# Optimization experiments

Measured on AMD Instinct MI355X. Metric: run time of the kernel, lower is better.

The kernel has to match this reference:

```python
import jax, jax.numpy as jnp
import numpy as np
from jax import lax

ITER, L, D, H = 8, 4096, 512, 256


def setup_inputs() -> dict:
    key = jax.random.key(0)
    ks = jax.random.split(key, 12)
    sD = 1.0 / np.sqrt(D)
    sH = 1.0 / np.sqrt(H)
    return {
        "embeddings_seq": jax.random.normal(ks[0], (ITER, L, D), jnp.float32),
        "ROIs": jax.random.uniform(ks[1], (1, L, 3), jnp.float32),
        "Wx": jax.random.normal(ks[2], (L, D), jnp.float32) * sD,
        "bx": jax.random.normal(ks[3], (L,), jnp.float32) * 0.01,
        "Wy": jax.random.normal(ks[4], (L, D), jnp.float32) * sD,
        "by": jax.random.normal(ks[5], (L,), jnp.float32) * 0.01,
        "Wz": jax.random.normal(ks[6], (L, D), jnp.float32) * sD,
        "bz": jax.random.normal(ks[7], (L,), jnp.float32) * 0.01,
        "Ws": jax.random.normal(ks[8], (D, H), jnp.float32) * sD,
        "bs": jax.random.normal(ks[9], (H,), jnp.float32) * 0.01,
        "Wh": jax.random.normal(ks[10], (L, H), jnp.float32) * sH,
        "bh": jax.random.normal(ks[11], (L,), jnp.float32) * 0.01,
    }


def reference(embeddings_seq, ROIs, Wx, bx, Wy, by, Wz, bz, Ws, bs, Wh, bh):
    # size_tensor = [1/767, 1/767, 1/575]
    size = jnp.array([1.0 / 767, 1.0 / 767, 1.0 / 575], dtype=embeddings_seq.dtype)

    def dec(h):  # grouped Conv1d(k=D, groups=L) == per-landmark dot product; h: [L, D]
        x = jnp.sum(Wx * h, axis=-1) + bx
        y = jnp.sum(Wy * h, axis=-1) + by
        z = jnp.sum(Wz * h, axis=-1) + bz
        return jnp.stack([x, y, z], axis=-1)  # [L, 3]

    def gate_head(h):  # Linear+Tanh shared, then per-landmark grouped conv; h: [L, D]
        s = jnp.tanh(h @ Ws + bs)          # [L, H]
        return jnp.sum(Wh * s, axis=-1) + bh  # [L]

    emb0 = embeddings_seq[0]                  # [L, D]
    rois0 = ROIs[0]                           # [L, 3]
    predict0 = dec(emb0) * size + rois0       # [L, 3]

    def step(carry, emb):
        h, c, pred = carry
        rois = pred                           # previous prediction becomes new ROIs
        gf = gate_head(h)                     # [L]
        ga = gate_head(emb)                   # [L]
        g = jax.nn.softmax(jnp.stack([gf, ga], axis=-1), axis=-1)  # [L, 2]
        g0, g1 = g[:, 0:1], g[:, 1:2]
        h = h * g0 + emb * g1
        c = c * g0 + rois * g1
        pred = dec(h) * size + lax.stop_gradient(c)
        return (h, c, pred), pred

    init = (emb0, rois0, predict0)
    _, preds = lax.scan(step, init, embeddings_seq[1:])  # [ITER-1, L, 3]
    return jnp.concatenate([predict0[None], preds], axis=0)  # [ITER, L, 3]
```

## Files before the change

### kernel.cpp

```cpp
#include <hip/hip_runtime.h>
#include <stdint.h>

#define L_DIM 4096
#define D_DIM 512
#define H_DIM 256
#define T_DIM 8

typedef short bf16x8 __attribute__((ext_vector_type(8)));
typedef float f32x4 __attribute__((ext_vector_type(4)));

__device__ __forceinline__ unsigned short f2bf(float f) {
    union { float f; unsigned int u; } c; c.f = f;
    unsigned int u = c.u;
    unsigned int r = (u + 0x7fffu + ((u >> 16) & 1u)) >> 16;
    return (unsigned short)r;
}

__device__ __forceinline__ float bits2f(unsigned int u) {
    union { unsigned int u; float f; } c; c.u = u; return c.f;
}

__device__ __forceinline__ float4 unpack_bf4(uint2 q) {
    float4 r;
    r.x = bits2f(q.x << 16);
    r.y = bits2f(q.x & 0xffff0000u);
    r.z = bits2f(q.y << 16);
    r.w = bits2f(q.y & 0xffff0000u);
    return r;
}

__device__ __forceinline__ float wave_sum(float x) {
    #pragma unroll
    for (int off = 32; off > 0; off >>= 1) x += __shfl_xor(x, off, 64);
    return x;
}

__device__ __forceinline__ float dot4(float4 a, float4 b) {
    return a.x * b.x + a.y * b.y + a.z * b.z + a.w * b.w;
}

__device__ __forceinline__ float fast_tanh(float x) {
    float e = __expf(2.0f * x);
    return 1.0f - 2.0f / (e + 1.0f);
}

__device__ __forceinline__ float4 tanh4b(float4 a, float4 b) {
    float4 r;
    r.x = fast_tanh(a.x + b.x); r.y = fast_tanh(a.y + b.y);
    r.z = fast_tanh(a.z + b.z); r.w = fast_tanh(a.w + b.w);
    return r;
}

__global__ void k_transpose_ws(const float* __restrict__ Ws,
                               unsigned short* __restrict__ WsT) {
    int idx = blockIdx.x * 256 + threadIdx.x;
    int j = idx >> 9;
    int k = idx & 511;
    WsT[idx] = f2bf(Ws[k * H_DIM + j]);
}

__global__ __launch_bounds__(512, 4) void k_fused(
    const float* __restrict__ emb, const float* __restrict__ rois,
    const float* __restrict__ Wx, const float* __restrict__ bx,
    const float* __restrict__ Wy, const float* __restrict__ by,
    const float* __restrict__ Wz, const float* __restrict__ bz,
    const float* __restrict__ bs, const float* __restrict__ Wh,
    const float* __restrict__ bh, const unsigned short* __restrict__ WsT,
    float* __restrict__ out) {
    __shared__ __align__(16) char smem[81920];

    const int tid  = threadIdx.x;
    const int lane = tid & 63;
    const int wid  = tid >> 6;
    const int wm   = wid >> 2;
    const int wn   = wid & 3;
    const int lbase = blockIdx.x * 8;

    const int arow = tid >> 4, aq = tid & 15;
    const int t0 = arow >> 3, li0 = arow & 7;
    const float* ag0 = emb + ((long)t0 * L_DIM + lbase + li0) * D_DIM + aq * 4;
    const float* ag1 = ag0 + (long)4 * L_DIM * D_DIM;
    const int adst0 = arow * 128 + ((aq * 8) ^ ((arow & 7) << 4));
    const int adst1 = (arow + 32) * 128 + ((aq * 8) ^ (((arow + 32) & 7) << 4));
    const int bj = tid >> 3, bko = tid & 7;
    const unsigned short* bg = WsT + (long)bj * D_DIM + bko * 8;
    const int bdst[4] = {
        bj * 128 + ((bko * 16) ^ ((bj & 7) << 4)),
        (bj + 64) * 128 + ((bko * 16) ^ (((bj + 64) & 7) << 4)),
        (bj + 128) * 128 + ((bko * 16) ^ (((bj + 128) & 7) << 4)),
        (bj + 192) * 128 + ((bko * 16) ^ (((bj + 192) & 7) << 4))};

    f32x4 acc[2][4];
    #pragma unroll
    for (int mi = 0; mi < 2; mi++)
        #pragma unroll
        for (int ni = 0; ni < 4; ni++) acc[mi][ni] = (f32x4){0.f, 0.f, 0.f, 0.f};

    {
        float4 a0 = *(const float4*)(ag0);
        float4 a1 = *(const float4*)(ag1);
        char* As = smem;
        char* Bs = smem + 8192;
        uint2 p0, p1;
        p0.x = (unsigned)f2bf(a0.x) | ((unsigned)f2bf(a0.y) << 16);
        p0.y = (unsigned)f2bf(a0.z) | ((unsigned)f2bf(a0.w) << 16);
        p1.x = (unsigned)f2bf(a1.x) | ((unsigned)f2bf(a1.y) << 16);
        p1.y = (unsigned)f2bf(a1.z) | ((unsigned)f2bf(a1.w) << 16);
        *(uint2*)(As + adst0) = p0;
        *(uint2*)(As + adst1) = p1;
        #pragma unroll
        for (int p = 0; p < 4; p++)
            *(uint4*)(Bs + bdst[p]) = *(const uint4*)(bg + (long)p * 64 * D_DIM);
    }
    __syncthreads();

    #pragma unroll
    for (int kt = 0; kt < 8; ++kt) {
        char* As = smem + (kt & 1) * 40960;
        char* Bs = As + 8192;
        char* Asn = smem + ((kt + 1) & 1) * 40960;
        char* Bsn = Asn + 8192;

        float4 a0, a1;
        uint4 b0, b1, b2, b3;
        if (kt < 7) {
            const float* ap0 = ag0 + (kt + 1) * 64;
            const float* ap1 = ag1 + (kt + 1) * 64;
            a0 = *(const float4*)(ap0);
            a1 = *(const float4*)(ap1);
            const unsigned short* bp = bg + (kt + 1) * 64;
            b0 = *(const uint4*)(bp);
            b1 = *(const uint4*)(bp + (long)64 * D_DIM);
            b2 = *(const uint4*)(bp + (long)128 * D_DIM);
            b3 = *(const uint4*)(bp + (long)192 * D_DIM);
        }

        #pragma unroll
        for (int ks = 0; ks < 2; ++ks) {
            bf16x8 a[2], b[4];
            #pragma unroll
            for (int mi = 0; mi < 2; mi++) {
                int row = wm * 32 + mi * 16 + (lane & 15);
                a[mi] = *(const bf16x8*)(As + row * 128 +
                          (((ks * 64) + (lane >> 4) * 16) ^ ((row & 7) << 4)));
            }
            #pragma unroll
            for (int ni = 0; ni < 4; ni++) {
                int j = wn * 64 + ni * 16 + (lane & 15);
                b[ni] = *(const bf16x8*)(Bs + j * 128 +
                          (((ks * 64) + (lane >> 4) * 16) ^ ((j & 7) << 4)));
            }
            #pragma unroll
            for (int mi = 0; mi < 2; mi++)
                #pragma unroll
                for (int ni = 0; ni < 4; ni++)
                    acc[mi][ni] = __builtin_amdgcn_mfma_f32_16x16x32_bf16(
                        a[mi], b[ni], acc[mi][ni], 0, 0, 0);
        }

        if (kt < 7) {
            uint2 p0, p1;
            p0.x = (unsigned)f2bf(a0.x) | ((unsigned)f2bf(a0.y) << 16);
            p0.y = (unsigned)f2bf(a0.z) | ((unsigned)f2bf(a0.w) << 16);
            p1.x = (unsigned)f2bf(a1.x) | ((unsigned)f2bf(a1.y) << 16);
            p1.y = (unsigned)f2bf(a1.z) | ((unsigned)f2bf(a1.w) << 16);
            *(uint2*)(Asn + adst0) = p0;
            *(uint2*)(Asn + adst1) = p1;
            *(uint4*)(Bsn + bdst[0]) = b0;
            *(uint4*)(Bsn + bdst[1]) = b1;
            *(uint4*)(Bsn + bdst[2]) = b2;
            *(uint4*)(Bsn + bdst[3]) = b3;
        }
        __syncthreads();
    }

    unsigned short* v_lds = (unsigned short*)smem;
    #pragma unroll
    for (int mi = 0; mi < 2; mi++)
        #pragma unroll
        for (int ni = 0; ni < 4; ni++)
            #pragma unroll
            for (int r = 0; r < 4; r++) {
                int row = wm * 32 + mi * 16 + (lane >> 4) * 4 + r;
                int col = wn * 64 + ni * 16 + (lane & 15);
                v_lds[row * H_DIM + col] = f2bf(acc[mi][ni][r]);
            }
    __syncthreads();

    const int l = lbase + wid;
    const int j4 = lane * 4;
    const int d8 = lane * 8;

    float4 Wh4 = *(const float4*)(Wh + (long)l * H_DIM + j4);
    float4 bs4 = *(const float4*)(bs + j4);
    float4 wx0 = *(const float4*)(Wx + (long)l * D_DIM + d8);
    float4 wx1 = *(const float4*)(Wx + (long)l * D_DIM + d8 + 4);
    float4 wy0 = *(const float4*)(Wy + (long)l * D_DIM + d8);
    float4 wy1 = *(const float4*)(Wy + (long)l * D_DIM + d8 + 4);
    float4 wz0 = *(const float4*)(Wz + (long)l * D_DIM + d8);
    float4 wz1 = *(const float4*)(Wz + (long)l * D_DIM + d8 + 4);
    float bxl = bx[l], byl = by[l], bzl = bz[l], bhl = bh[l];
    const float sx = 1.f / 767.f, sy = 1.f / 767.f, sz = 1.f / 575.f;

    uint2 vvp[T_DIM];
    #pragma unroll
    for (int t = 0; t < T_DIM; ++t)
        vvp[t] = *(const uint2*)(v_lds + (t * 8 + wid) * H_DIM + j4);

    float px[T_DIM], py[T_DIM], pz[T_DIM], ga[T_DIM];
    #pragma unroll
    for (int t = 0; t < T_DIM; ++t) {
        const float* eb = emb + ((long)t * L_DIM + l) * D_DIM + d8;
        float4 f0 = *(const float4*)(eb);
        float4 f1 = *(const float4*)(eb + 4);
        px[t] = dot4(wx0, f0) + dot4(wx1, f1);
        py[t] = dot4(wy0, f0) + dot4(wy1, f1);
        pz[t] = dot4(wz0, f0) + dot4(wz1, f1);
        float4 sa = tanh4b(unpack_bf4(vvp[t]), bs4);
        ga[t] = dot4(Wh4, sa);
    }
    #pragma unroll
    for (int t = 0; t < T_DIM; ++t) {
        px[t] = wave_sum(px[t]);
        py[t] = wave_sum(py[t]);
        pz[t] = wave_sum(pz[t]);
        ga[t] = wave_sum(ga[t]) + bhl;
    }

    float4 u4 = unpack_bf4(vvp[0]);
    float cx = rois[l * 3 + 0], cy = rois[l * 3 + 1], cz = rois[l * 3 + 2];
    float dx = px[0], dy = py[0], dz = pz[0];
    float prx = (dx + bxl) * sx + cx;
    float pry = (dy + byl) * sy + cy;
    float prz = (dz + bzl) * sz + cz;
    if (lane == 0) {
        out[l * 3 + 0] = prx; out[l * 3 + 1] = pry; out[l * 3 + 2] = prz;
    }

    #pragma unroll
    for (int t = 1; t < T_DIM; ++t) {
        float4 sf = tanh4b(u4, bs4);
        float gf = wave_sum(dot4(Wh4, sf)) + bhl;

        float g0 = 1.0f / (1.0f + __expf(ga[t] - gf));
        float g1 = 1.0f - g0;

        float4 v4 = unpack_bf4(vvp[t]);
        u4.x = g0 * u4.x + g1 * v4.x; u4.y = g0 * u4.y + g1 * v4.y;
        u4.z = g0 * u4.z + g1 * v4.z; u4.w = g0 * u4.w + g1 * v4.w;

        cx = cx * g0 + prx * g1; cy = cy * g0 + pry * g1; cz = cz * g0 + prz * g1;
        dx = g0 * dx + g1 * px[t]; dy = g0 * dy + g1 * py[t]; dz = g0 * dz + g1 * pz[t];

        prx = (dx + bxl) * sx + cx;
        pry = (dy + byl) * sy + cy;
        prz = (dz + bzl) * sz + cz;
        if (lane == 0) {
            float* o = out + (long)t * (L_DIM * 3) + l * 3;
            o[0] = prx; o[1] = pry; o[2] = prz;
        }
    }
}

extern "C" void kernel_launch(void* const* d_in, const int* in_sizes, int n_in,
                              void* d_out, int out_size, void* d_ws, size_t ws_size,
                              hipStream_t stream) {
    const float* emb  = (const float*)d_in[0];
    const float* rois = (const float*)d_in[1];
    const float* Wx   = (const float*)d_in[2];
    const float* bx   = (const float*)d_in[3];
    const float* Wy   = (const float*)d_in[4];
    const float* by   = (const float*)d_in[5];
    const float* Wz   = (const float*)d_in[6];
    const float* bz   = (const float*)d_in[7];
    const float* Ws   = (const float*)d_in[8];
    const float* bs   = (const float*)d_in[9];
    const float* Wh   = (const float*)d_in[10];
    const float* bh   = (const float*)d_in[11];
    float* out = (float*)d_out;

    unsigned short* WsT = (unsigned short*)d_ws;

    hipLaunchKernelGGL(k_transpose_ws, dim3(512), dim3(256), 0, stream, Ws, WsT);
    hipLaunchKernelGGL(k_fused, dim3(512), dim3(512), 0, stream,
                       emb, rois, Wx, bx, Wy, by, Wz, bz, bs, Wh, bh, WsT, out);
}
```

Baseline: 153.8 us.

## Stage full bf16 embedding tile in LDS and reuse it for decoder dot products

The kernel now loads each block's whole 64x512 embedding tile into LDS as bf16 up front, instead of streaming it per k-step alongside the Ws tile. The epilogue reads these bf16 values from LDS rather than re-reading fp32 embeddings from global memory. This removes the second global pass over the embeddings. In exchange, LDS grows to 128KB, which allows fewer resident blocks per CU. The A-operand load is no longer overlapped with compute, and the decoder and gating math now use bf16-rounded embeddings, which lowers precision.

```diff
diff --git a/kernel.cpp b/kernel.cpp
--- a/kernel.cpp
+++ b/kernel.cpp
@@ -14,6 +14,10 @@
     unsigned int u = c.u;
     unsigned int r = (u + 0x7fffu + ((u >> 16) & 1u)) >> 16;
     return (unsigned short)r;
+}
+
+__device__ __forceinline__ unsigned int pack2(float a, float b) {
+    return (unsigned)f2bf(a) | ((unsigned)f2bf(b) << 16);
 }
 
 __device__ __forceinline__ float bits2f(unsigned int u) {
@@ -59,7 +63,7 @@
     WsT[idx] = f2bf(Ws[k * H_DIM + j]);
 }
 
-__global__ __launch_bounds__(512, 4) void k_fused(
+__global__ __launch_bounds__(512, 2) void k_fused(
     const float* __restrict__ emb, const float* __restrict__ rois,
     const float* __restrict__ Wx, const float* __restrict__ bx,
     const float* __restrict__ Wy, const float* __restrict__ by,
@@ -67,7 +71,7 @@
     const float* __restrict__ bs, const float* __restrict__ Wh,
     const float* __restrict__ bh, const unsigned short* __restrict__ WsT,
     float* __restrict__ out) {
-    __shared__ __align__(16) char smem[81920];
+    __shared__ __align__(16) char smem[131072];
 
     const int tid  = threadIdx.x;
     const int lane = tid & 63;
@@ -76,12 +80,6 @@
     const int wn   = wid & 3;
     const int lbase = blockIdx.x * 8;
 
-    const int arow = tid >> 4, aq = tid & 15;
-    const int t0 = arow >> 3, li0 = arow & 7;
-    const float* ag0 = emb + ((long)t0 * L_DIM + lbase + li0) * D_DIM + aq * 4;
-    const float* ag1 = ag0 + (long)4 * L_DIM * D_DIM;
-    const int adst0 = arow * 128 + ((aq * 8) ^ ((arow & 7) << 4));
-    const int adst1 = (arow + 32) * 128 + ((aq * 8) ^ (((arow + 32) & 7) << 4));
     const int bj = tid >> 3, bko = tid & 7;
     const unsigned short* bg = WsT + (long)bj * D_DIM + bko * 8;
     const int bdst[4] = {
@@ -90,44 +88,46 @@
         (bj + 128) * 128 + ((bko * 16) ^ (((bj + 128) & 7) << 4)),
         (bj + 192) * 128 + ((bko * 16) ^ (((bj + 192) & 7) << 4))};
 
+    {
+        const int row = tid >> 3;
+        const int oct = tid & 7;
+        const int t0 = row >> 3, li0 = row & 7;
+        const float* asrc = emb + ((long)t0 * L_DIM + lbase + li0) * D_DIM + oct * 64;
+        float4 ebuf[16];
+        #pragma unroll
+        for (int q = 0; q < 16; ++q) ebuf[q] = *(const float4*)(asrc + q * 4);
+
+        char* Bs0 = smem + 65536;
+        #pragma unroll
+        for (int p = 0; p < 4; p++)
+            *(uint4*)(Bs0 + bdst[p]) = *(const uint4*)(bg + (long)p * 64 * D_DIM);
+
+        const int row7 = (row & 7) << 4;
+        #pragma unroll
+        for (int c = 0; c < 8; ++c) {
+            uint4 w;
+            w.x = pack2(ebuf[2 * c].x, ebuf[2 * c].y);
+            w.y = pack2(ebuf[2 * c].z, ebuf[2 * c].w);
+            w.z = pack2(ebuf[2 * c + 1].x, ebuf[2 * c + 1].y);
+            w.w = pack2(ebuf[2 * c + 1].z, ebuf[2 * c + 1].w);
+            *(uint4*)(smem + row * 1024 + ((((oct * 8 + c) * 16)) ^ row7)) = w;
+        }
+    }
+    __syncthreads();
+
     f32x4 acc[2][4];
     #pragma unroll
     for (int mi = 0; mi < 2; mi++)
         #pragma unroll
         for (int ni = 0; ni < 4; ni++) acc[mi][ni] = (f32x4){0.f, 0.f, 0.f, 0.f};
 
-    {
-        float4 a0 = *(const float4*)(ag0);
-        float4 a1 = *(const float4*)(ag1);
-        char* As = smem;
-        char* Bs = smem + 8192;
-        uint2 p0, p1;
-        p0.x = (unsigned)f2bf(a0.x) | ((unsigned)f2bf(a0.y) << 16);
-        p0.y = (unsigned)f2bf(a0.z) | ((unsigned)f2bf(a0.w) << 16);
-        p1.x = (unsigned)f2bf(a1.x) | ((unsigned)f2bf(a1.y) << 16);
-        p1.y = (unsigned)f2bf(a1.z) | ((unsigned)f2bf(a1.w) << 16);
-        *(uint2*)(As + adst0) = p0;
-        *(uint2*)(As + adst1) = p1;
-        #pragma unroll
-        for (int p = 0; p < 4; p++)
-            *(uint4*)(Bs + bdst[p]) = *(const uint4*)(bg + (long)p * 64 * D_DIM);
-    }
-    __syncthreads();
-
     #pragma unroll
     for (int kt = 0; kt < 8; ++kt) {
-        char* As = smem + (kt & 1) * 40960;
-        char* Bs = As + 8192;
-        char* Asn = smem + ((kt + 1) & 1) * 40960;
-        char* Bsn = Asn + 8192;
-
-        float4 a0, a1;
+        char* Bs  = smem + 65536 + (kt & 1) * 32768;
+        char* Bsn = smem + 65536 + ((kt + 1) & 1) * 32768;
+
         uint4 b0, b1, b2, b3;
         if (kt < 7) {
-            const float* ap0 = ag0 + (kt + 1) * 64;
-            const float* ap1 = ag1 + (kt + 1) * 64;
-            a0 = *(const float4*)(ap0);
-            a1 = *(const float4*)(ap1);
             const unsigned short* bp = bg + (kt + 1) * 64;
             b0 = *(const uint4*)(bp);
             b1 = *(const uint4*)(bp + (long)64 * D_DIM);
@@ -141,8 +141,9 @@
             #pragma unroll
             for (int mi = 0; mi < 2; mi++) {
                 int row = wm * 32 + mi * 16 + (lane & 15);
-                a[mi] = *(const bf16x8*)(As + row * 128 +
-                          (((ks * 64) + (lane >> 4) * 16) ^ ((row & 7) << 4)));
+                int chunk = kt * 8 + ks * 4 + (lane >> 4);
+                a[mi] = *(const bf16x8*)(smem + row * 1024 +
+                          ((chunk * 16) ^ ((row & 7) << 4)));
             }
             #pragma unroll
             for (int ni = 0; ni < 4; ni++) {
@@ -159,13 +160,6 @@
         }
 
         if (kt < 7) {
-            uint2 p0, p1;
-            p0.x = (unsigned)f2bf(a0.x) | ((unsigned)f2bf(a0.y) << 16);
-            p0.y = (unsigned)f2bf(a0.z) | ((unsigned)f2bf(a0.w) << 16);
-            p1.x = (unsigned)f2bf(a1.x) | ((unsigned)f2bf(a1.y) << 16);
-            p1.y = (unsigned)f2bf(a1.z) | ((unsigned)f2bf(a1.w) << 16);
-            *(uint2*)(Asn + adst0) = p0;
-            *(uint2*)(Asn + adst1) = p1;
             *(uint4*)(Bsn + bdst[0]) = b0;
             *(uint4*)(Bsn + bdst[1]) = b1;
             *(uint4*)(Bsn + bdst[2]) = b2;
@@ -174,7 +168,7 @@
         __syncthreads();
     }
 
-    unsigned short* v_lds = (unsigned short*)smem;
+    unsigned short* v_lds = (unsigned short*)(smem + 65536);
     #pragma unroll
     for (int mi = 0; mi < 2; mi++)
         #pragma unroll
@@ -189,10 +183,10 @@
 
     const int l = lbase + wid;
     const int j4 = lane * 4;
-    const int d8 = lane * 8;
 
     float4 Wh4 = *(const float4*)(Wh + (long)l * H_DIM + j4);
     float4 bs4 = *(const float4*)(bs + j4);
+    const int d8 = lane * 8;
     float4 wx0 = *(const float4*)(Wx + (long)l * D_DIM + d8);
     float4 wx1 = *(const float4*)(Wx + (long)l * D_DIM + d8 + 4);
     float4 wy0 = *(const float4*)(Wy + (long)l * D_DIM + d8);
@@ -210,9 +204,11 @@
     float px[T_DIM], py[T_DIM], pz[T_DIM], ga[T_DIM];
     #pragma unroll
     for (int t = 0; t < T_DIM; ++t) {
-        const float* eb = emb + ((long)t * L_DIM + l) * D_DIM + d8;
-        float4 f0 = *(const float4*)(eb);
-        float4 f1 = *(const float4*)(eb + 4);
+        int r = t * 8 + wid;
+        uint4 ev = *(const uint4*)(smem + r * 1024 +
+                     ((lane * 16) ^ ((r & 7) << 4)));
+        float4 f0 = unpack_bf4(make_uint2(ev.x, ev.y));
+        float4 f1 = unpack_bf4(make_uint2(ev.z, ev.w));
         px[t] = dot4(wx0, f0) + dot4(wx1, f1);
         py[t] = dot4(wy0, f0) + dot4(wy1, f1);
         pz[t] = dot4(wz0, f0) + dot4(wz1, f1);
```

Measured after the change: 160.2 us. 4.1% more time.

## Fuse xyz decoder dot products into GEMM A-tile load and single-buffer Ws

Applied to the files above, without the earlier changes.

Computes the Wx/Wy/Wz per-landmark dot products from the fp32 embedding values already loaded for the GEMM A tile, so the second full read of the embeddings in the epilogue is removed. Partial sums are reduced over 16-lane groups and passed through LDS. The Ws B tile becomes single-buffered with an extra barrier per k-step, which cuts LDS use from 80KB to 48KB so more blocks can be resident per CU. The cost is two barriers per iteration, extra global loads of Wx/Wy/Wz inside the main loop, and a changed fp32 summation order for the decoder outputs.

```diff
diff --git a/kernel.cpp b/kernel.cpp
--- a/kernel.cpp
+++ b/kernel.cpp
@@ -14,6 +14,10 @@
     unsigned int u = c.u;
     unsigned int r = (u + 0x7fffu + ((u >> 16) & 1u)) >> 16;
     return (unsigned short)r;
+}
+
+__device__ __forceinline__ unsigned int pack2(float a, float b) {
+    return (unsigned)f2bf(a) | ((unsigned)f2bf(b) << 16);
 }
 
 __device__ __forceinline__ float bits2f(unsigned int u) {
@@ -32,6 +36,12 @@
 __device__ __forceinline__ float wave_sum(float x) {
     #pragma unroll
     for (int off = 32; off > 0; off >>= 1) x += __shfl_xor(x, off, 64);
+    return x;
+}
+
+__device__ __forceinline__ float group16_sum(float x) {
+    #pragma unroll
+    for (int off = 8; off > 0; off >>= 1) x += __shfl_xor(x, off, 64);
     return x;
 }
 
@@ -67,7 +77,8 @@
     const float* __restrict__ bs, const float* __restrict__ Wh,
     const float* __restrict__ bh, const unsigned short* __restrict__ WsT,
     float* __restrict__ out) {
-    __shared__ __align__(16) char smem[81920];
+    __shared__ __align__(16) char smem[49152];
+    char* Bs = smem + 16384;
 
     const int tid  = threadIdx.x;
     const int lane = tid & 63;
@@ -82,6 +93,10 @@
     const float* ag1 = ag0 + (long)4 * L_DIM * D_DIM;
     const int adst0 = arow * 128 + ((aq * 8) ^ ((arow & 7) << 4));
     const int adst1 = (arow + 32) * 128 + ((aq * 8) ^ (((arow + 32) & 7) << 4));
+    const float* wxg = Wx + (long)(lbase + li0) * D_DIM + aq * 4;
+    const float* wyg = Wy + (long)(lbase + li0) * D_DIM + aq * 4;
+    const float* wzg = Wz + (long)(lbase + li0) * D_DIM + aq * 4;
+
     const int bj = tid >> 3, bko = tid & 7;
     const unsigned short* bg = WsT + (long)bj * D_DIM + bko * 8;
     const int bdst[4] = {
@@ -90,6 +105,9 @@
         (bj + 128) * 128 + ((bko * 16) ^ (((bj + 128) & 7) << 4)),
         (bj + 192) * 128 + ((bko * 16) ^ (((bj + 192) & 7) << 4))};
 
+    float pxa0 = 0.f, pya0 = 0.f, pza0 = 0.f;
+    float pxa1 = 0.f, pya1 = 0.f, pza1 = 0.f;
+
     f32x4 acc[2][4];
     #pragma unroll
     for (int mi = 0; mi < 2; mi++)
@@ -99,40 +117,41 @@
     {
         float4 a0 = *(const float4*)(ag0);
         float4 a1 = *(const float4*)(ag1);
-        char* As = smem;
-        char* Bs = smem + 8192;
-        uint2 p0, p1;
-        p0.x = (unsigned)f2bf(a0.x) | ((unsigned)f2bf(a0.y) << 16);
-        p0.y = (unsigned)f2bf(a0.z) | ((unsigned)f2bf(a0.w) << 16);
-        p1.x = (unsigned)f2bf(a1.x) | ((unsigned)f2bf(a1.y) << 16);
-        p1.y = (unsigned)f2bf(a1.z) | ((unsigned)f2bf(a1.w) << 16);
-        *(uint2*)(As + adst0) = p0;
-        *(uint2*)(As + adst1) = p1;
+        float4 wx = *(const float4*)(wxg);
+        float4 wy = *(const float4*)(wyg);
+        float4 wz = *(const float4*)(wzg);
         #pragma unroll
         for (int p = 0; p < 4; p++)
             *(uint4*)(Bs + bdst[p]) = *(const uint4*)(bg + (long)p * 64 * D_DIM);
+        pxa0 += dot4(wx, a0); pya0 += dot4(wy, a0); pza0 += dot4(wz, a0);
+        pxa1 += dot4(wx, a1); pya1 += dot4(wy, a1); pza1 += dot4(wz, a1);
+        uint2 p0, p1;
+        p0.x = pack2(a0.x, a0.y); p0.y = pack2(a0.z, a0.w);
+        p1.x = pack2(a1.x, a1.y); p1.y = pack2(a1.z, a1.w);
+        *(uint2*)(smem + adst0) = p0;
+        *(uint2*)(smem + adst1) = p1;
     }
     __syncthreads();
 
     #pragma unroll
     for (int kt = 0; kt < 8; ++kt) {
-        char* As = smem + (kt & 1) * 40960;
-        char* Bs = As + 8192;
-        char* Asn = smem + ((kt + 1) & 1) * 40960;
-        char* Bsn = Asn + 8192;
-
-        float4 a0, a1;
+        char* As  = smem + (kt & 1) * 8192;
+        char* Asn = smem + ((kt + 1) & 1) * 8192;
+
+        float4 a0, a1, wx, wy, wz;
         uint4 b0, b1, b2, b3;
         if (kt < 7) {
-            const float* ap0 = ag0 + (kt + 1) * 64;
-            const float* ap1 = ag1 + (kt + 1) * 64;
-            a0 = *(const float4*)(ap0);
-            a1 = *(const float4*)(ap1);
-            const unsigned short* bp = bg + (kt + 1) * 64;
+            const int o = (kt + 1) * 64;
+            a0 = *(const float4*)(ag0 + o);
+            a1 = *(const float4*)(ag1 + o);
+            const unsigned short* bp = bg + o;
             b0 = *(const uint4*)(bp);
             b1 = *(const uint4*)(bp + (long)64 * D_DIM);
             b2 = *(const uint4*)(bp + (long)128 * D_DIM);
             b3 = *(const uint4*)(bp + (long)192 * D_DIM);
+            wx = *(const float4*)(wxg + o);
+            wy = *(const float4*)(wyg + o);
+            wz = *(const float4*)(wzg + o);
         }
 
         #pragma unroll
@@ -159,22 +178,26 @@
         }
 
         if (kt < 7) {
+            pxa0 += dot4(wx, a0); pya0 += dot4(wy, a0); pza0 += dot4(wz, a0);
+            pxa1 += dot4(wx, a1); pya1 += dot4(wy, a1); pza1 += dot4(wz, a1);
             uint2 p0, p1;
-            p0.x = (unsigned)f2bf(a0.x) | ((unsigned)f2bf(a0.y) << 16);
-            p0.y = (unsigned)f2bf(a0.z) | ((unsigned)f2bf(a0.w) << 16);
-            p1.x = (unsigned)f2bf(a1.x) | ((unsigned)f2bf(a1.y) << 16);
-            p1.y = (unsigned)f2bf(a1.z) | ((unsigned)f2bf(a1.w) << 16);
+            p0.x = pack2(a0.x, a0.y); p0.y = pack2(a0.z, a0.w);
+            p1.x = pack2(a1.x, a1.y); p1.y = pack2(a1.z, a1.w);
             *(uint2*)(Asn + adst0) = p0;
             *(uint2*)(Asn + adst1) = p1;
-            *(uint4*)(Bsn + bdst[0]) = b0;
-            *(uint4*)(Bsn + bdst[1]) = b1;
-            *(uint4*)(Bsn + bdst[2]) = b2;
-            *(uint4*)(Bsn + bdst[3]) = b3;
         }
         __syncthreads();
-    }
-
-    unsigned short* v_lds = (unsigned short*)smem;
+        if (kt < 7) {
+            *(uint4*)(Bs + bdst[0]) = b0;
+            *(uint4*)(Bs + bdst[1]) = b1;
+            *(uint4*)(Bs + bdst[2]) = b2;
+            *(uint4*)(Bs + bdst[3]) = b3;
+        }
+        __syncthreads();
+    }
+
+    unsigned short* v_lds = (unsigned short*)(smem + 16384);
+    float* p_lds = (float*)smem;
     #pragma unroll
     for (int mi = 0; mi < 2; mi++)
         #pragma unroll
@@ -185,47 +208,40 @@
                 int col = wn * 64 + ni * 16 + (lane & 15);
                 v_lds[row * H_DIM + col] = f2bf(acc[mi][ni][r]);
             }
+    pxa0 = group16_sum(pxa0); pya0 = group16_sum(pya0); pza0 = group16_sum(pza0);
+    pxa1 = group16_sum(pxa1); pya1 = group16_sum(pya1); pza1 = group16_sum(pza1);
+    if ((lane & 15) == 0) {
+        p_lds[arow * 4 + 0] = pxa0;
+        p_lds[arow * 4 + 1] = pya0;
+        p_lds[arow * 4 + 2] = pza0;
+        p_lds[(arow + 32) * 4 + 0] = pxa1;
+        p_lds[(arow + 32) * 4 + 1] = pya1;
+        p_lds[(arow + 32) * 4 + 2] = pza1;
+    }
     __syncthreads();
 
     const int l = lbase + wid;
     const int j4 = lane * 4;
-    const int d8 = lane * 8;
 
     float4 Wh4 = *(const float4*)(Wh + (long)l * H_DIM + j4);
     float4 bs4 = *(const float4*)(bs + j4);
-    float4 wx0 = *(const float4*)(Wx + (long)l * D_DIM + d8);
-    float4 wx1 = *(const float4*)(Wx + (long)l * D_DIM + d8 + 4);
-    float4 wy0 = *(const float4*)(Wy + (long)l * D_DIM + d8);
-    float4 wy1 = *(const float4*)(Wy + (long)l * D_DIM + d8 + 4);
-    float4 wz0 = *(const float4*)(Wz + (long)l * D_DIM + d8);
-    float4 wz1 = *(const float4*)(Wz + (long)l * D_DIM + d8 + 4);
     float bxl = bx[l], byl = by[l], bzl = bz[l], bhl = bh[l];
     const float sx = 1.f / 767.f, sy = 1.f / 767.f, sz = 1.f / 575.f;
 
     uint2 vvp[T_DIM];
-    #pragma unroll
-    for (int t = 0; t < T_DIM; ++t)
-        vvp[t] = *(const uint2*)(v_lds + (t * 8 + wid) * H_DIM + j4);
-
     float px[T_DIM], py[T_DIM], pz[T_DIM], ga[T_DIM];
     #pragma unroll
     for (int t = 0; t < T_DIM; ++t) {
-        const float* eb = emb + ((long)t * L_DIM + l) * D_DIM + d8;
-        float4 f0 = *(const float4*)(eb);
-        float4 f1 = *(const float4*)(eb + 4);
-        px[t] = dot4(wx0, f0) + dot4(wx1, f1);
-        py[t] = dot4(wy0, f0) + dot4(wy1, f1);
-        pz[t] = dot4(wz0, f0) + dot4(wz1, f1);
+        int r = t * 8 + wid;
+        vvp[t] = *(const uint2*)(v_lds + r * H_DIM + j4);
+        px[t] = p_lds[r * 4 + 0];
+        py[t] = p_lds[r * 4 + 1];
+        pz[t] = p_lds[r * 4 + 2];
         float4 sa = tanh4b(unpack_bf4(vvp[t]), bs4);
         ga[t] = dot4(Wh4, sa);
     }
     #pragma unroll
-    for (int t = 0; t < T_DIM; ++t) {
-        px[t] = wave_sum(px[t]);
-        py[t] = wave_sum(py[t]);
-        pz[t] = wave_sum(pz[t]);
-        ga[t] = wave_sum(ga[t]) + bhl;
-    }
+    for (int t = 0; t < T_DIM; ++t) ga[t] = wave_sum(ga[t]) + bhl;
 
     float4 u4 = unpack_bf4(vvp[0]);
     float cx = rois[l * 3 + 0], cy = rois[l * 3 + 1], cz = rois[l * 3 + 2];
```

Measured after the change: 193.7 us. 1.26x slower.

## Single-buffer the Ws tile in LDS to cut shared memory and raise occupancy

Applied to the files above, without the earlier changes.

Cuts the LDS footprint from 80KB to 48KB by double-buffering only the activation tile and keeping a single buffer for the transposed Ws tile. Each k-step now needs an extra barrier before the next Ws tile is written. The launch bound changes from 4 to 6 blocks, which allows more resident blocks but tightens the register budget and risks spills. The load of the bf16 projection from LDS is moved into the per-timestep loop so it interleaves with the global embedding loads.

```diff
diff --git a/kernel.cpp b/kernel.cpp
--- a/kernel.cpp
+++ b/kernel.cpp
@@ -14,6 +14,10 @@
     unsigned int u = c.u;
     unsigned int r = (u + 0x7fffu + ((u >> 16) & 1u)) >> 16;
     return (unsigned short)r;
+}
+
+__device__ __forceinline__ unsigned int pack2(float a, float b) {
+    return (unsigned)f2bf(a) | ((unsigned)f2bf(b) << 16);
 }
 
 __device__ __forceinline__ float bits2f(unsigned int u) {
@@ -59,7 +63,7 @@
     WsT[idx] = f2bf(Ws[k * H_DIM + j]);
 }
 
-__global__ __launch_bounds__(512, 4) void k_fused(
+__global__ __launch_bounds__(512, 6) void k_fused(
     const float* __restrict__ emb, const float* __restrict__ rois,
     const float* __restrict__ Wx, const float* __restrict__ bx,
     const float* __restrict__ Wy, const float* __restrict__ by,
@@ -67,7 +71,8 @@
     const float* __restrict__ bs, const float* __restrict__ Wh,
     const float* __restrict__ bh, const unsigned short* __restrict__ WsT,
     float* __restrict__ out) {
-    __shared__ __align__(16) char smem[81920];
+    __shared__ __align__(16) char smem[49152];
+    char* Bs = smem + 16384;
 
     const int tid  = threadIdx.x;
     const int lane = tid & 63;
@@ -82,6 +87,7 @@
     const float* ag1 = ag0 + (long)4 * L_DIM * D_DIM;
     const int adst0 = arow * 128 + ((aq * 8) ^ ((arow & 7) << 4));
     const int adst1 = (arow + 32) * 128 + ((aq * 8) ^ (((arow + 32) & 7) << 4));
+
     const int bj = tid >> 3, bko = tid & 7;
     const unsigned short* bg = WsT + (long)bj * D_DIM + bko * 8;
     const int bdst[4] = {
@@ -99,36 +105,29 @@
     {
         float4 a0 = *(const float4*)(ag0);
         float4 a1 = *(const float4*)(ag1);
-        char* As = smem;
-        char* Bs = smem + 8192;
-        uint2 p0, p1;
-        p0.x = (unsigned)f2bf(a0.x) | ((unsigned)f2bf(a0.y) << 16);
-        p0.y = (unsigned)f2bf(a0.z) | ((unsigned)f2bf(a0.w) << 16);
-        p1.x = (unsigned)f2bf(a1.x) | ((unsigned)f2bf(a1.y) << 16);
-        p1.y = (unsigned)f2bf(a1.z) | ((unsigned)f2bf(a1.w) << 16);
-        *(uint2*)(As + adst0) = p0;
-        *(uint2*)(As + adst1) = p1;
         #pragma unroll
         for (int p = 0; p < 4; p++)
             *(uint4*)(Bs + bdst[p]) = *(const uint4*)(bg + (long)p * 64 * D_DIM);
+        uint2 p0, p1;
+        p0.x = pack2(a0.x, a0.y); p0.y = pack2(a0.z, a0.w);
+        p1.x = pack2(a1.x, a1.y); p1.y = pack2(a1.z, a1.w);
+        *(uint2*)(smem + adst0) = p0;
+        *(uint2*)(smem + adst1) = p1;
     }
     __syncthreads();
 
     #pragma unroll
     for (int kt = 0; kt < 8; ++kt) {
-        char* As = smem + (kt & 1) * 40960;
-        char* Bs = As + 8192;
-        char* Asn = smem + ((kt + 1) & 1) * 40960;
-        char* Bsn = Asn + 8192;
+        char* As  = smem + (kt & 1) * 8192;
+        char* Asn = smem + ((kt + 1) & 1) * 8192;
 
         float4 a0, a1;
         uint4 b0, b1, b2, b3;
         if (kt < 7) {
-            const float* ap0 = ag0 + (kt + 1) * 64;
-            const float* ap1 = ag1 + (kt + 1) * 64;
-            a0 = *(const float4*)(ap0);
-            a1 = *(const float4*)(ap1);
-            const unsigned short* bp = bg + (kt + 1) * 64;
+            const int o = (kt + 1) * 64;
+            a0 = *(const float4*)(ag0 + o);
+            a1 = *(const float4*)(ag1 + o);
+            const unsigned short* bp = bg + o;
             b0 = *(const uint4*)(bp);
             b1 = *(const uint4*)(bp + (long)64 * D_DIM);
             b2 = *(const uint4*)(bp + (long)128 * D_DIM);
@@ -160,21 +159,22 @@
 
         if (kt < 7) {
             uint2 p0, p1;
-            p0.x = (unsigned)f2bf(a0.x) | ((unsigned)f2bf(a0.y) << 16);
-            p0.y = (unsigned)f2bf(a0.z) | ((unsigned)f2bf(a0.w) << 16);
-            p1.x = (unsigned)f2bf(a1.x) | ((unsigned)f2bf(a1.y) << 16);
-            p1.y = (unsigned)f2bf(a1.z) | ((unsigned)f2bf(a1.w) << 16);
+            p0.x = pack2(a0.x, a0.y); p0.y = pack2(a0.z, a0.w);
+            p1.x = pack2(a1.x, a1.y); p1.y = pack2(a1.z, a1.w);
             *(uint2*)(Asn + adst0) = p0;
             *(uint2*)(Asn + adst1) = p1;
-            *(uint4*)(Bsn + bdst[0]) = b0;
-            *(uint4*)(Bsn + bdst[1]) = b1;
-            *(uint4*)(Bsn + bdst[2]) = b2;
-            *(uint4*)(Bsn + bdst[3]) = b3;
         }
         __syncthreads();
-    }
-
-    unsigned short* v_lds = (unsigned short*)smem;
+        if (kt < 7) {
+            *(uint4*)(Bs + bdst[0]) = b0;
+            *(uint4*)(Bs + bdst[1]) = b1;
+            *(uint4*)(Bs + bdst[2]) = b2;
+            *(uint4*)(Bs + bdst[3]) = b3;
+        }
+        __syncthreads();
+    }
+
+    unsigned short* v_lds = (unsigned short*)(smem + 16384);
     #pragma unroll
     for (int mi = 0; mi < 2; mi++)
         #pragma unroll
@@ -203,10 +203,6 @@
     const float sx = 1.f / 767.f, sy = 1.f / 767.f, sz = 1.f / 575.f;
 
     uint2 vvp[T_DIM];
-    #pragma unroll
-    for (int t = 0; t < T_DIM; ++t)
-        vvp[t] = *(const uint2*)(v_lds + (t * 8 + wid) * H_DIM + j4);
-
     float px[T_DIM], py[T_DIM], pz[T_DIM], ga[T_DIM];
     #pragma unroll
     for (int t = 0; t < T_DIM; ++t) {
@@ -216,6 +212,7 @@
         px[t] = dot4(wx0, f0) + dot4(wx1, f1);
         py[t] = dot4(wy0, f0) + dot4(wy1, f1);
         pz[t] = dot4(wz0, f0) + dot4(wz1, f1);
+        vvp[t] = *(const uint2*)(v_lds + (t * 8 + wid) * H_DIM + j4);
         float4 sa = tanh4b(unpack_bf4(vvp[t]), bs4);
         ga[t] = dot4(Wh4, sa);
     }
```

Result: slower. 216.8 us (+41.0%).
